# Kernel optimization log

Hardware: AMD Instinct MI355X
Metric: run time of the kernel (lower is better)

## Reference

```python
import jax, jax.numpy as jnp
import numpy as np

B, T, D = 1, 1024, 256
NH, MULT = 4, 32
N = MULT * D // NH          # 2048 sparse dim per head
CS = 256                    # rotary chunk size
V, VP = 50257, 50304        # vocab, padded vocab
L = 4                       # n_layer (single shared BDHLayer applied L times)
GATE_DIV = 1024.0
CHUNK = 64                  # GLA chunk size
ROPE_BASE = 2.0 ** 18
SCALE_BASE = 512.0


def sqrelu(x):
    return jnp.square(jax.nn.relu(x))


def rmsnorm(x, eps=1e-5):
    return x * jax.lax.rsqrt(jnp.mean(jnp.square(x), -1, keepdims=True) + eps)


def layernorm(x, eps=1e-5):
    m = jnp.mean(x, -1, keepdims=True)
    v = jnp.var(x, -1, keepdims=True)
    return (x - m) * jax.lax.rsqrt(v + eps)


def rope_tables(t_len):
    # flash-attn RotaryEmbedding with xpos scale_base (q branch)
    inv_freq = 1.0 / (ROPE_BASE ** (jnp.arange(0, CS, 2, dtype=jnp.float32) / CS))
    t = jnp.arange(t_len, dtype=jnp.float32)
    freqs = t[:, None] * inv_freq[None, :]                       # [T, CS/2]
    xpos_scale = (jnp.arange(0, CS, 2, dtype=jnp.float32) + 0.4 * CS) / (1.4 * CS)
    power = (t - t_len // 2) / SCALE_BASE
    sc = xpos_scale[None, :] ** power[:, None]
    return jnp.cos(freqs) * sc, jnp.sin(freqs) * sc


def apply_rope(x, cos, sin):
    # x: [B, T, nchunks, CS]; non-interleaved rotation of full CS dim
    half = CS // 2
    x1, x2 = x[..., :half], x[..., half:]
    c = cos[None, :, None, :]
    s = sin[None, :, None, :]
    return jnp.concatenate([x1 * c - x2 * s, x2 * c + x1 * s], axis=-1)


def chunk_gla(q, k, v, g):
    # Gated linear attention: S_t = exp(g_t)[:,None]*S_{t-1} + k_t v_t^T; o_t = scale*q_t @ S_t
    # q,k,g: [B,T,H,N] (g = log decay <= 0), v: [B,T,H,Dv]. Chunked, IO-aware form.
    Bq, Tq, H, Nk = q.shape
    Dv = v.shape[-1]
    nc = Tq // CHUNK
    scale = Nk ** -0.5  # fla default scale = K**-0.5

    def to_chunks(x):
        return x.reshape(Bq, nc, CHUNK, H, -1).transpose(1, 0, 3, 2, 4)  # [nc,B,H,C,*]

    qc, kc, vc, gc = to_chunks(q), to_chunks(k), to_chunks(v), to_chunks(g)
    mask = jnp.tril(jnp.ones((CHUNK, CHUNK), dtype=q.dtype))

    def step(S, inp):
        qb, kb, vb, gb = inp                              # [B,H,C,N], v: [B,H,C,Dv]
        gcs = jnp.cumsum(gb, axis=2)                      # inclusive cumulative log-decay
        qg = qb * jnp.exp(gcs) * scale
        A = jnp.einsum('bhtn,bhsn->bhts', qg, kb * jnp.exp(-gcs))
        o = jnp.einsum('bhts,bhsd->bhtd', A * mask, vb)   # intra-chunk
        o = o + jnp.einsum('bhtn,bhnd->bhtd', qg, S)      # inter-chunk
        g_last = gcs[:, :, -1, :]                         # [B,H,N]
        kS = kb * jnp.exp(g_last[:, :, None, :] - gcs)
        S = S * jnp.exp(g_last)[..., None] + jnp.einsum('bhtn,bhtd->bhnd', kS, vb)
        return S, o

    S0 = jnp.zeros((Bq, H, Nk, Dv), dtype=q.dtype)
    _, outs = jax.lax.scan(step, S0, (qc, kc, vc, gc))    # outs: [nc,B,H,C,Dv]
    return outs.transpose(1, 0, 3, 2, 4).reshape(Bq, Tq, H, Dv)


def bdh_layer(x, enc_w, enc_gate_w, dec_w, enc_v_w, cos, sin):
    Bx, Tx, Dx = x.shape
    xs = sqrelu(x @ enc_w.T)                              # [B,T,NH*N] sparse activations
    xr = apply_rope(xs.reshape(Bx, Tx, -1, CS), cos, sin)
    q = xr.reshape(Bx, Tx, NH, N)
    gate = sqrelu(x @ enc_gate_w.T).reshape(Bx, Tx, NH, N) / GATE_DIV
    v = jnp.broadcast_to(x[:, :, None, :], (Bx, Tx, NH, Dx))
    o = chunk_gla(q, q, v, -gate)                         # K = Q, g = -gate
    o = layernorm(o)                                      # middle_norm (no affine)
    ys = sqrelu(jnp.einsum('bthd,hnd->bthn', o, enc_v_w)) # per-head encoder_v
    xy = (xs.reshape(Bx, Tx, NH, N) * ys).reshape(Bx, Tx, NH * N)
    y = layernorm(xy @ dec_w.T)                           # end_norm (no affine)
    return rmsnorm(y + x)


def setup_inputs() -> dict:
    key = jax.random.key(0)
    ks = jax.random.split(key, 7)
    std = 0.02
    return {
        'embed_w': jax.random.normal(ks[0], (VP, D), jnp.float32) * std,
        'lm_head_w': jax.random.normal(ks[1], (VP, D), jnp.float32) * std,
        'enc_w': jax.random.normal(ks[2], (NH * N, D), jnp.float32) * std,
        'enc_gate_w': jax.random.normal(ks[3], (NH * N, D), jnp.float32) * std,
        'dec_w': jax.random.normal(ks[4], (D, NH * N), jnp.float32) * std,
        'enc_v_w': jax.random.normal(ks[5], (NH, N, D), jnp.float32) * std,
        'backout_lambda': 0.2 * jnp.ones((1,), jnp.float32),
        'resid_lambdas': jnp.ones((L,), jnp.float32),
        'x0_lambdas': jnp.zeros((L,), jnp.float32),
        'idx': jax.random.randint(ks[6], (B, T), 0, V, dtype=jnp.int32),
    }


def reference(embed_w, lm_head_w, enc_w, enc_gate_w, dec_w, enc_v_w,
              backout_lambda, resid_lambdas, x0_lambdas, idx):
    cos, sin = rope_tables(T)
    x = rmsnorm(embed_w[idx])                             # [B,T,D]
    x0 = x
    for i in range(L):                                    # single shared layer applied L times
        xin = resid_lambdas[i] * x + x0_lambdas[i] * x0
        x = bdh_layer(xin, enc_w, enc_gate_w, dec_w, enc_v_w, cos, sin)
    x = rmsnorm(x - backout_lambda * x0)                  # backout of embedding direction
    return x @ lm_head_w.T                                # logits [B,T,VP]
```

## Files before the change

kernel.cpp:

```cpp
#include <hip/hip_runtime.h>
#include <math.h>

#define TLEN 1024
#define DDIM 256
#define NH_  4
#define NDIM 2048
#define HN   8192
#define NCH  16
#define CHK  64
#define VP_  50304
#define SCALE_Q 0.022097086912079608f

typedef unsigned short u16;
typedef __attribute__((ext_vector_type(8))) short short8;
typedef __attribute__((ext_vector_type(4))) float f32x4;

#define MFMA16(a,b,c) __builtin_amdgcn_mfma_f32_16x16x32_bf16((a),(b),(c),0,0,0)

__device__ __forceinline__ float bf2f(u16 u){ return __uint_as_float(((unsigned)u)<<16); }
__device__ __forceinline__ u16 f2bf(float f){
  unsigned x = __float_as_uint(f);
  return (u16)((x + 0x7fffu + ((x>>16)&1u)) >> 16);
}
__device__ __forceinline__ float wave_sum(float v){
  #pragma unroll
  for(int o=1;o<64;o<<=1) v += __shfl_xor(v,o,64);
  return v;
}
__device__ __forceinline__ float block_sum(float v, float* tmp){
  v = wave_sum(v);
  __syncthreads();
  if((threadIdx.x&63)==0) tmp[threadIdx.x>>6]=v;
  __syncthreads();
  return tmp[0]+tmp[1]+tmp[2]+tmp[3];
}

__device__ __forceinline__ void gload16(const u16* g, u16* l){
  __builtin_amdgcn_global_load_lds((const __attribute__((address_space(1))) unsigned int*)g,
                                   (__attribute__((address_space(3))) unsigned int*)l, 16, 0, 0);
}
__device__ __forceinline__ short8 frag_lin(const u16* lds, int row, int k){
  return *(const short8*)((const char*)lds + row*128 + k*2);
}
__device__ __forceinline__ short8 frag64(const u16* lds, int row, int k){
  return *(const short8*)((const char*)lds + row*128 + ((k*2) ^ ((row&7)<<4)));
}
__device__ __forceinline__ short8 frag512(const u16* lds, int row, int k){
  return *(const short8*)((const char*)lds + row*512 + ((k*2) ^ ((row&7)<<4)));
}

__global__ __launch_bounds__(256) void k_setup(
  const float* __restrict__ emb, const int* __restrict__ idx,
  const float* rl, const float* xl,
  const float* __restrict__ enc_w, const float* __restrict__ gate_w,
  const float* __restrict__ dec_w, const float* __restrict__ encv_w,
  u16* w_enc, u16* w_gate, u16* w_dec, u16* w_encv,
  float* cosT, float* sinT, float* x0, float* xin, u16* xin_bf){
  __shared__ float tmp[4];
  int bid = blockIdx.x, tid = threadIdx.x;
  if(bid < 1024){
    if(tid < 128){
      int t = bid, i = tid;
      float inv_freq = exp2f(-18.0f * (float)(2*i) * (1.0f/256.0f));
      float fr = (float)t * inv_freq;
      float xsc = ((float)(2*i) + 102.4f) * (1.0f/358.4f);
      float power = ((float)t - 512.0f) * (1.0f/512.0f);
      float sc = exp2f(power * log2f(xsc));
      cosT[t*128+i] = cosf(fr)*sc;
      sinT[t*128+i] = sinf(fr)*sc;
    }
  } else if(bid < 5120){
    size_t base = (size_t)(bid-1024)*2048 + tid;
    #pragma unroll
    for(int k=0;k<8;k++){
      size_t i = base + (size_t)k*256;
      int seg = (int)(i>>21); size_t off = i & 2097151;
      const float* s; u16* dst;
      if(seg==0){ s=enc_w; dst=w_enc; } else if(seg==1){ s=gate_w; dst=w_gate; }
      else if(seg==2){ s=dec_w; dst=w_dec; } else { s=encv_w; dst=w_encv; }
      dst[off] = f2bf(s[off]);
    }
  } else {
    int t = bid - 5120, d = tid;
    float v = emb[(size_t)idx[t]*DDIM + d];
    float s = block_sum(v*v, tmp);
    float o = v * rsqrtf(s*(1.0f/DDIM) + 1e-5f);
    x0[t*DDIM+d] = o;
    float xi = rl[0]*o + xl[0]*o;
    xin[t*DDIM+d] = xi; xin_bf[t*DDIM+d] = f2bf(xi);
  }
}

template<bool SPLITK>
__global__ __launch_bounds__(256) void k_gemm(
  const u16* __restrict__ A, int lda, const u16* __restrict__ B, int ldb,
  float* __restrict__ C, int ldc, int kchunk)
{
  __shared__ __align__(16) u16 sA[128*64];
  __shared__ __align__(16) u16 sB[128*64];
  const int m0 = blockIdx.x*128, n0 = blockIdx.y*128;
  const int k0 = blockIdx.z*kchunk;
  const int tid = threadIdx.x, lane = tid&63, wv = tid>>6;
  const int wr = (wv>>1)*64, wc = (wv&1)*64;
  f32x4 acc[4][4];
  #pragma unroll
  for(int i=0;i<4;i++)
    #pragma unroll
    for(int j=0;j<4;j++) acc[i][j] = (f32x4){0.f,0.f,0.f,0.f};
  for(int kb=0; kb<kchunk; kb+=64){
    __syncthreads();
    #pragma unroll
    for(int p=0;p<4;p++){
      int r = p*32 + (tid>>3), cb = tid&7;
      int off = r*64 + cb*8;
      gload16(A + (size_t)(m0+r)*lda + k0+kb + cb*8, sA + off);
      gload16(B + (size_t)(n0+r)*ldb + k0+kb + cb*8, sB + off);
    }
    __syncthreads();
    #pragma unroll
    for(int ks=0;ks<2;ks++){
      short8 af[4], bfr[4];
      int kk = ks*32 + 8*(lane>>4);
      #pragma unroll
      for(int i=0;i<4;i++){
        af[i]  = frag_lin(sA, wr + i*16 + (lane&15), kk);
        bfr[i] = frag_lin(sB, wc + i*16 + (lane&15), kk);
      }
      #pragma unroll
      for(int i=0;i<4;i++)
        #pragma unroll
        for(int j=0;j<4;j++)
          acc[i][j] = MFMA16(af[i], bfr[j], acc[i][j]);
    }
  }
  size_t poff = SPLITK ? (size_t)blockIdx.z * (size_t)gridDim.x * 128 * ldc : 0;
  const int rb = 4*(lane>>4), cb2 = lane&15;
  #pragma unroll
  for(int i=0;i<4;i++)
    #pragma unroll
    for(int j=0;j<4;j++){
      int col = n0 + wc + j*16 + cb2;
      #pragma unroll
      for(int r=0;r<4;r++){
        int row = m0 + wr + i*16 + rb + r;
        C[poff + (size_t)row*ldc + col] = acc[i][j][r];
      }
    }
}

__global__ __launch_bounds__(256) void k_gemm_lm(
  const u16* __restrict__ A, const float* __restrict__ Bf, float* __restrict__ C)
{
  __shared__ __align__(16) u16 sB[128*256];
  __shared__ __align__(16) u16 sA[128*64];
  const int n0 = blockIdx.y*128, mbase = blockIdx.x*4;
  const int tid = threadIdx.x, lane = tid&63, wv = tid>>6;
  const int wr = (wv>>1)*64, wc = (wv&1)*64;
  {
    int n = tid>>1, half = tid&1;
    const float* bp = Bf + (size_t)(n0+n)*DDIM + half*128;
    #pragma unroll
    for(int s=0;s<16;s++){
      f32x4 v0 = *(const f32x4*)(bp + s*8);
      f32x4 v1 = *(const f32x4*)(bp + s*8 + 4);
      short8 w;
      #pragma unroll
      for(int e=0;e<4;e++){ w[e]=(short)f2bf(v0[e]); w[e+4]=(short)f2bf(v1[e]); }
      int k0 = half*128 + s*8;
      *(short8*)((char*)sB + n*512 + ((k0*2) ^ ((n&7)<<4))) = w;
    }
  }
  for(int mi=0; mi<4; mi++){
    int m0 = (mbase+mi)*128;
    f32x4 acc[4][4];
    #pragma unroll
    for(int i=0;i<4;i++)
      #pragma unroll
      for(int j=0;j<4;j++) acc[i][j] = (f32x4){0.f,0.f,0.f,0.f};
    for(int kb=0; kb<4; kb++){
      __syncthreads();
      #pragma unroll
      for(int p=0;p<4;p++){
        int r = p*32 + (tid>>3), cb = tid&7;
        gload16(A + (size_t)(m0+r)*DDIM + kb*64 + cb*8, sA + r*64 + cb*8);
      }
      __syncthreads();
      #pragma unroll
      for(int ks=0;ks<2;ks++){
        short8 af[4], bfr[4];
        int kk = ks*32 + 8*(lane>>4);
        #pragma unroll
        for(int i=0;i<4;i++){
          af[i]  = frag_lin(sA, wr + i*16 + (lane&15), kk);
          bfr[i] = frag512(sB, wc + i*16 + (lane&15), kb*64 + kk);
        }
        #pragma unroll
        for(int i=0;i<4;i++)
          #pragma unroll
          for(int j=0;j<4;j++)
            acc[i][j] = MFMA16(af[i], bfr[j], acc[i][j]);
      }
    }
    const int rb = 4*(lane>>4), cb2 = lane&15;
    #pragma unroll
    for(int i=0;i<4;i++)
      #pragma unroll
      for(int j=0;j<4;j++){
        int col = n0 + wc + j*16 + cb2;
        #pragma unroll
        for(int r=0;r<4;r++){
          int row = m0 + wr + i*16 + rb + r;
          C[(size_t)row*VP_ + col] = acc[i][j][r];
        }
      }
  }
}

__global__ __launch_bounds__(256) void k_gemm_eg(
  const u16* __restrict__ xin_bf, const u16* __restrict__ w_enc, const u16* __restrict__ w_gate,
  u16* __restrict__ xs, u16* __restrict__ gate)
{
  __shared__ __align__(16) u16 sA[128*64];
  __shared__ __align__(16) u16 sB[128*64];
  const int yy = blockIdx.y;
  const bool isg = yy >= 64;
  const u16* B = isg ? w_gate : w_enc;
  u16* C = isg ? gate : xs;
  const float mul = isg ? (1.0f/1024.0f) : 1.0f;
  const int m0 = blockIdx.x*128, n0 = (yy&63)*128;
  const int tid = threadIdx.x, lane = tid&63, wv = tid>>6;
  const int wr = (wv>>1)*64, wc = (wv&1)*64;
  f32x4 acc[4][4];
  #pragma unroll
  for(int i=0;i<4;i++)
    #pragma unroll
    for(int j=0;j<4;j++) acc[i][j] = (f32x4){0.f,0.f,0.f,0.f};
  for(int kb=0; kb<DDIM; kb+=64){
    __syncthreads();
    #pragma unroll
    for(int p=0;p<4;p++){
      int r = p*32 + (tid>>3), cb = tid&7;
      int off = r*64 + cb*8;
      gload16(xin_bf + (size_t)(m0+r)*DDIM + kb + cb*8, sA + off);
      gload16(B + (size_t)(n0+r)*DDIM + kb + cb*8, sB + off);
    }
    __syncthreads();
    #pragma unroll
    for(int ks=0;ks<2;ks++){
      short8 af[4], bfr[4];
      int kk = ks*32 + 8*(lane>>4);
      #pragma unroll
      for(int i=0;i<4;i++){
        af[i]  = frag_lin(sA, wr + i*16 + (lane&15), kk);
        bfr[i] = frag_lin(sB, wc + i*16 + (lane&15), kk);
      }
      #pragma unroll
      for(int i=0;i<4;i++)
        #pragma unroll
        for(int j=0;j<4;j++)
          acc[i][j] = MFMA16(af[i], bfr[j], acc[i][j]);
    }
  }
  const int rb = 4*(lane>>4), cb2 = lane&15;
  #pragma unroll
  for(int i=0;i<4;i++)
    #pragma unroll
    for(int j=0;j<4;j++){
      int col = n0 + wc + j*16 + cb2;
      #pragma unroll
      for(int r=0;r<4;r++){
        int row = m0 + wr + i*16 + rb + r;
        float v = acc[i][j][r];
        float a = v>0.f ? v*v*mul : 0.f;
        C[(size_t)row*HN + col] = f2bf(a);
      }
    }
}

__global__ __launch_bounds__(256) void k_gemm_ys(
  const u16* __restrict__ olnp, const u16* __restrict__ wvp,
  const u16* __restrict__ xs, u16* __restrict__ xy)
{
  __shared__ __align__(16) u16 sA[128*64];
  __shared__ __align__(16) u16 sB[128*64];
  const int m0 = blockIdx.x*128, n0 = blockIdx.y*128, h = blockIdx.z;
  const u16* A = olnp + (size_t)h*TLEN*DDIM;
  const u16* B = wvp  + (size_t)h*NDIM*DDIM;
  const int tid = threadIdx.x, lane = tid&63, wv = tid>>6;
  const int wr = (wv>>1)*64, wc = (wv&1)*64;
  f32x4 acc[4][4];
  #pragma unroll
  for(int i=0;i<4;i++)
    #pragma unroll
    for(int j=0;j<4;j++) acc[i][j] = (f32x4){0.f,0.f,0.f,0.f};
  for(int kb=0; kb<DDIM; kb+=64){
    __syncthreads();
    #pragma unroll
    for(int p=0;p<4;p++){
      int r = p*32 + (tid>>3), cb = tid&7;
      int off = r*64 + cb*8;
      gload16(A + (size_t)(m0+r)*DDIM + kb + cb*8, sA + off);
      gload16(B + (size_t)(n0+r)*DDIM + kb + cb*8, sB + off);
    }
    __syncthreads();
    #pragma unroll
    for(int ks=0;ks<2;ks++){
      short8 af[4], bfr[4];
      int kk = ks*32 + 8*(lane>>4);
      #pragma unroll
      for(int i=0;i<4;i++){
        af[i]  = frag_lin(sA, wr + i*16 + (lane&15), kk);
        bfr[i] = frag_lin(sB, wc + i*16 + (lane&15), kk);
      }
      #pragma unroll
      for(int i=0;i<4;i++)
        #pragma unroll
        for(int j=0;j<4;j++)
          acc[i][j] = MFMA16(af[i], bfr[j], acc[i][j]);
    }
  }
  const int rb = 4*(lane>>4), cb2 = lane&15;
  #pragma unroll
  for(int i=0;i<4;i++)
    #pragma unroll
    for(int j=0;j<4;j++){
      int col = h*NDIM + n0 + wc + j*16 + cb2;
      #pragma unroll
      for(int r=0;r<4;r++){
        int row = m0 + wr + i*16 + rb + r;
        float v = acc[i][j][r];
        float a = v>0.f ? v*v : 0.f;
        a *= bf2f(xs[(size_t)row*HN + col]);
        xy[(size_t)row*HN + col] = f2bf(a);
      }
    }
}

__global__ __launch_bounds__(256) void k_phase_a(const u16* __restrict__ xs, u16* __restrict__ gate,
                          const float* __restrict__ cosT, const float* __restrict__ sinT,
                          u16* __restrict__ qg, u16* __restrict__ kgT, float* __restrict__ gle,
                          const u16* __restrict__ xin_bf, u16* __restrict__ vbT){
  __shared__ u16 s[64*DDIM];
  int c = blockIdx.y;
  if(blockIdx.x == 32){
    int tid = threadIdx.x;
    #pragma unroll
    for(int p=0;p<8;p++){
      int idx = p*256+tid; int t = idx>>5, cb = idx&31;
      *(short8*)(s + t*DDIM + cb*8) = *(const short8*)(xin_bf + ((size_t)c*CHK + t)*DDIM + cb*8);
    }
    __syncthreads();
    int d = tid;
    u16 col[64];
    #pragma unroll
    for(int t=0;t<64;t++) col[t] = s[t*DDIM + d];
    u16* dst = vbT + ((size_t)c*DDIM + d)*CHK;
    #pragma unroll
    for(int p=0;p<8;p++){
      short8 v;
      #pragma unroll
      for(int e=0;e<8;e++) v[e] = (short)col[p*8+e];
      *(short8*)(dst + p*8) = v;
    }
    return;
  }
  int j = blockIdx.x*256 + threadIdx.x;
  int h = j>>11, n = j&2047;
  int cc = j & 255;
  int ci = cc & 127;
  bool hi_ = cc >= 128;
  int poff = hi_ ? -128 : 128;
  size_t base = (size_t)c*CHK*HN + j;
  float gsum = 0.f;
  #pragma unroll
  for(int t=0;t<CHK;t++) gsum -= bf2f(gate[base + (size_t)t*HN]);
  float egsum = expf(gsum);
  u16 kv[64];
  float gc = 0.f;
  #pragma unroll
  for(int t=0;t<CHK;t++){
    size_t ix = base + (size_t)t*HN;
    gc -= bf2f(gate[ix]);
    int tt = c*CHK + t;
    float own = bf2f(xs[ix]), oth = bf2f(xs[ix + poff]);
    float cs = cosT[tt*128+ci], sn = sinT[tt*128+ci];
    float qv = hi_ ? (own*cs + oth*sn) : (own*cs - oth*sn);
    float e1 = expf(gc);
    qg[ix] = f2bf(qv * e1 * SCALE_Q);
    u16 kgv = f2bf(qv / e1);
    gate[ix] = kgv;
    kv[t] = kgv;
  }
  u16* kb = kgT + (((size_t)c*NH_ + h)*NDIM + n)*CHK;
  #pragma unroll
  for(int p=0;p<8;p++){
    short8 v;
    #pragma unroll
    for(int e=0;e<8;e++) v[e] = (short)kv[p*8+e];
    *(short8*)(kb + p*8) = v;
  }
  gle[(size_t)c*HN + j] = egsum;
}

__global__ __launch_bounds__(256) void k_qk_part(const u16* __restrict__ qg, const u16* __restrict__ kg,
                                                 float* __restrict__ Apart){
  int c = blockIdx.x, h = blockIdx.y, kz = blockIdx.z;
  int tid = threadIdx.x, lane = tid&63, wv = tid>>6;
  __shared__ __align__(16) u16 sQ[2][64*64], sK[2][64*64];
  const u16* qb = qg + (size_t)c*CHK*HN + h*NDIM + kz*512;
  const u16* kb = kg + (size_t)c*CHK*HN + h*NDIM + kz*512;
  f32x4 acc[4];
  #pragma unroll
  for(int j=0;j<4;j++) acc[j] = (f32x4){0.f,0.f,0.f,0.f};
  #pragma unroll
  for(int p=0;p<2;p++){
    int r = p*32 + (tid>>3), cb = tid&7;
    int off = r*64 + cb*8;
    gload16(qb + (size_t)r*HN + cb*8, sQ[0] + off);
    gload16(kb + (size_t)r*HN + cb*8, sK[0] + off);
  }
  __syncthreads();
  for(int kt=0; kt<8; kt++){
    if(kt<7){
      #pragma unroll
      for(int p=0;p<2;p++){
        int r = p*32 + (tid>>3), cb = tid&7;
        int off = r*64 + cb*8;
        gload16(qb + (kt+1)*64 + (size_t)r*HN + cb*8, sQ[(kt+1)&1] + off);
        gload16(kb + (kt+1)*64 + (size_t)r*HN + cb*8, sK[(kt+1)&1] + off);
      }
    }
    #pragma unroll
    for(int kh=0;kh<2;kh++){
      int kk = kh*32 + 8*(lane>>4);
      short8 af = frag_lin(sQ[kt&1], wv*16 + (lane&15), kk);
      #pragma unroll
      for(int j=0;j<4;j++){
        short8 b = frag_lin(sK[kt&1], j*16 + (lane&15), kk);
        acc[j] = MFMA16(af, b, acc[j]);
      }
    }
    __syncthreads();
  }
  int rb = 4*(lane>>4), cl = lane&15;
  float* ab = Apart + (size_t)kz*(NCH*NH_*4096) + ((size_t)c*NH_+h)*4096;
  #pragma unroll
  for(int j=0;j<4;j++)
    #pragma unroll
    for(int r=0;r<4;r++){
      int t = wv*16 + rb + r, s = j*16 + cl;
      ab[t*64 + s] = acc[j][r];
    }
}

__global__ __launch_bounds__(256) void k_state(const u16* __restrict__ kgT, const u16* __restrict__ vbT,
                                               const float* __restrict__ gle, u16* __restrict__ ST){
  int nb = blockIdx.x, db = blockIdx.y, h = blockIdx.z;
  int tid = threadIdx.x, lane = tid&63, wv = tid>>6;
  __shared__ __align__(16) u16 sK[2][32*64], sV[2][64*64];
  __shared__ __align__(16) u16 sD[64*32];
  int ng = nb*32;
  int r8a = tid>>3, cb = tid&7;
  f32x4 S[2];
  S[0] = (f32x4){0.f,0.f,0.f,0.f}; S[1] = (f32x4){0.f,0.f,0.f,0.f};
  gload16(kgT + (((size_t)0*NH_ + h)*NDIM + ng + r8a)*CHK + cb*8, sK[0] + r8a*64 + cb*8);
  #pragma unroll
  for(int p=0;p<2;p++){
    int r = p*32 + r8a;
    gload16(vbT + ((size_t)0*DDIM + db*64 + r)*CHK + cb*8, sV[0] + r*64 + cb*8);
  }
  int cur = 0;
  for(int c=0;c<15;c++){
    __syncthreads();
    if(c<14){
      gload16(kgT + (((size_t)(c+1)*NH_ + h)*NDIM + ng + r8a)*CHK + cb*8, sK[cur^1] + r8a*64 + cb*8);
      #pragma unroll
      for(int p=0;p<2;p++){
        int r = p*32 + r8a;
        gload16(vbT + ((size_t)(c+1)*DDIM + db*64 + r)*CHK + cb*8, sV[cur^1] + r*64 + cb*8);
      }
    }
    #pragma unroll
    for(int kh=0;kh<2;kh++){
      int kk = kh*32 + 8*(lane>>4);
      short8 af = frag_lin(sV[cur], wv*16 + (lane&15), kk);
      #pragma unroll
      for(int fn=0;fn<2;fn++){
        short8 b = frag_lin(sK[cur], fn*16 + (lane&15), kk);
        S[fn] = MFMA16(af, b, S[fn]);
      }
    }
    #pragma unroll
    for(int fn=0;fn<2;fn++){
      float gv = gle[(size_t)c*HN + h*NDIM + ng + fn*16 + (lane&15)];
      S[fn][0]*=gv; S[fn][1]*=gv; S[fn][2]*=gv; S[fn][3]*=gv;
    }
    #pragma unroll
    for(int fn=0;fn<2;fn++)
      #pragma unroll
      for(int r=0;r<4;r++){
        int d = wv*16 + 4*(lane>>4) + r, n = fn*16 + (lane&15);
        *(u16*)((char*)sD + d*64 + ((n*2) ^ (((d>>2)&3)<<4))) = f2bf(S[fn][r]);
      }
    __syncthreads();
    {
      int dl = tid>>2, seg = tid&3;
      short8 v = *(const short8*)((const char*)sD + dl*64 + ((seg*16) ^ (((dl>>2)&3)<<4)));
      *(short8*)(ST + (((size_t)c*NH_ + h)*DDIM + db*64 + dl)*NDIM + ng + seg*8) = v;
    }
    cur ^= 1;
  }
}

__global__ __launch_bounds__(256) void k_out(const u16* __restrict__ qg, const u16* __restrict__ ST,
                                             const float* __restrict__ Apart, const u16* __restrict__ vbT,
                                             float* __restrict__ op){
  int c = blockIdx.x, h = blockIdx.y, zz = blockIdx.z;
  int db = zz>>1, nz = zz&1;
  int tid = threadIdx.x, lane = tid&63, wv = tid>>6;
  __shared__ __align__(16) u16 sQ[2][64*64], sS[2][64*64];
  __shared__ __align__(16) u16 sAm[64*64], sV[64*64];
  const u16* stb = (c>0) ? ST + ((size_t)(c-1)*NH_ + h)*DDIM*(size_t)NDIM + (size_t)db*64*NDIM : ST;
  const u16* qb  = qg + (size_t)c*CHK*HN + h*NDIM;
  const int ktA = nz ? 15 : 0, ktB = nz ? 32 : 15;
  int r8a = tid>>3, cb = tid&7;
  f32x4 acc[4];
  #pragma unroll
  for(int j=0;j<4;j++) acc[j] = (f32x4){0.f,0.f,0.f,0.f};
  if(c>0){
    #pragma unroll
    for(int p=0;p<2;p++){
      int r = p*32 + r8a;
      gload16(qb + ktA*64 + (size_t)r*HN + cb*8, sQ[0] + r*64 + cb*8);
      gload16(stb + (size_t)r*NDIM + ktA*64 + cb*8, sS[0] + r*64 + cb*8);
    }
  }
  if(nz==0){
    size_t abase = ((size_t)c*NH_ + h)*4096;
    #pragma unroll
    for(int e=0;e<16;e++){
      int idx = e*256 + tid;
      int t = idx>>6, s = idx&63;
      float sum = Apart[abase + idx]
                + Apart[(size_t)(NCH*NH_*4096)   + abase + idx]
                + Apart[(size_t)(NCH*NH_*4096)*2 + abase + idx]
                + Apart[(size_t)(NCH*NH_*4096)*3 + abase + idx];
      *(u16*)((char*)sAm + t*128 + ((s*2)^((t&7)<<4))) = f2bf((s<=t)? sum : 0.f);
    }
    #pragma unroll
    for(int p=0;p<2;p++){
      int r = p*32 + r8a;
      gload16(vbT + ((size_t)c*DDIM + db*64 + r)*CHK + cb*8, sV + r*64 + cb*8);
    }
  }
  __syncthreads();
  if(nz==0){
    #pragma unroll
    for(int kh=0;kh<2;kh++){
      int kk = kh*32 + 8*(lane>>4);
      short8 af = frag64(sAm, wv*16 + (lane&15), kk);
      #pragma unroll
      for(int j=0;j<4;j++){
        short8 b = frag_lin(sV, j*16 + (lane&15), kk);
        acc[j] = MFMA16(af, b, acc[j]);
      }
    }
  }
  if(c>0){
    int cur = 0;
    for(int kt=ktA; kt<ktB; kt++){
      if(kt+1<ktB){
        #pragma unroll
        for(int p=0;p<2;p++){
          int r = p*32 + r8a;
          gload16(qb + (kt+1)*64 + (size_t)r*HN + cb*8, sQ[cur^1] + r*64 + cb*8);
          gload16(stb + (size_t)r*NDIM + (kt+1)*64 + cb*8, sS[cur^1] + r*64 + cb*8);
        }
      }
      #pragma unroll
      for(int kh=0;kh<2;kh++){
        int kk = kh*32 + 8*(lane>>4);
        short8 af = frag_lin(sQ[cur], wv*16 + (lane&15), kk);
        #pragma unroll
        for(int j=0;j<4;j++){
          short8 b = frag_lin(sS[cur], j*16 + (lane&15), kk);
          acc[j] = MFMA16(af, b, acc[j]);
        }
      }
      __syncthreads();
      cur ^= 1;
    }
  }
  int rb = 4*(lane>>4), cl = lane&15;
  #pragma unroll
  for(int j=0;j<4;j++){
    int d = db*64 + j*16 + cl;
    #pragma unroll
    for(int r=0;r<4;r++){
      int t = c*CHK + wv*16 + rb + r;
      op[((size_t)(nz*NH_ + h)*TLEN + t)*DDIM + d] = acc[j][r];
    }
  }
}

__global__ __launch_bounds__(256) void k_ln(const float* __restrict__ op, u16* __restrict__ oln){
  __shared__ float tmp[4];
  int t = blockIdx.x, h = blockIdx.y, d = threadIdx.x;
  size_t ix = ((size_t)h*TLEN + t)*DDIM + d;
  float v = op[ix] + op[(size_t)NH_*TLEN*DDIM + ix];
  float s1 = block_sum(v, tmp);
  float m = s1*(1.0f/DDIM);
  float cv = v - m;
  float s2 = block_sum(cv*cv, tmp);
  oln[ix] = f2bf(cv * rsqrtf(s2*(1.0f/DDIM) + 1e-5f));
}

__global__ __launch_bounds__(256) void k_post(const float* __restrict__ ypart, float* __restrict__ xin,
                                              const float* __restrict__ x0,
                                              const float* rl, const float* xl, const float* bl,
                                              int li, u16* __restrict__ xin_bf, u16* __restrict__ xf){
  __shared__ float tmp[4];
  int t = blockIdx.x, d = threadIdx.x;
  float v = 0.f;
  #pragma unroll
  for(int z=0;z<16;z++) v += ypart[(size_t)z*TLEN*DDIM + t*DDIM + d];
  float s1 = block_sum(v, tmp);
  float m = s1*(1.0f/DDIM);
  float cvt = v - m;
  float s2 = block_sum(cvt*cvt, tmp);
  float y = cvt * rsqrtf(s2*(1.0f/DDIM) + 1e-5f);
  float xn = y + xin[t*DDIM+d];
  float s3 = block_sum(xn*xn, tmp);
  float xv = xn * rsqrtf(s3*(1.0f/DDIM) + 1e-5f);
  if(li<3){
    float xi = rl[li+1]*xv + xl[li+1]*x0[t*DDIM+d];
    xin[t*DDIM+d] = xi; xin_bf[t*DDIM+d] = f2bf(xi);
  } else {
    float fv = xv - bl[0]*x0[t*DDIM+d];
    float s4 = block_sum(fv*fv, tmp);
    xf[t*DDIM+d] = f2bf(fv * rsqrtf(s4*(1.0f/DDIM) + 1e-5f));
  }
}

extern "C" void kernel_launch(void* const* d_in, const int* in_sizes, int n_in,
                              void* d_out, int out_size, void* d_ws, size_t ws_size,
                              hipStream_t stream){
  (void)in_sizes; (void)n_in; (void)out_size; (void)ws_size;
  const float* embed_w = (const float*)d_in[0];
  const float* lm_w    = (const float*)d_in[1];
  const float* enc_w   = (const float*)d_in[2];
  const float* gate_w  = (const float*)d_in[3];
  const float* dec_w   = (const float*)d_in[4];
  const float* encv_w  = (const float*)d_in[5];
  const float* backout = (const float*)d_in[6];
  const float* rlam    = (const float*)d_in[7];
  const float* xlam    = (const float*)d_in[8];
  const int*   idx     = (const int*)d_in[9];
  float* out = (float*)d_out;

  char* p = (char*)d_ws;
  auto alloc = [&](size_t b)->char*{ char* r=p; p += (b+255)&~(size_t)255; return r; };
  float* cosT = (float*)alloc((size_t)TLEN*128*4);
  float* sinT = (float*)alloc((size_t)TLEN*128*4);
  float* x0   = (float*)alloc((size_t)TLEN*DDIM*4);
  float* xin  = (float*)alloc((size_t)TLEN*DDIM*4);
  u16* xin_bf = (u16*)alloc((size_t)TLEN*DDIM*2);
  u16* xs     = (u16*)alloc((size_t)TLEN*HN*2);
  u16* q      = (u16*)alloc((size_t)TLEN*HN*2);
  u16* gate   = (u16*)alloc((size_t)TLEN*HN*2);
  (void)alloc((size_t)15*NH_*DDIM*NDIM*2 - (size_t)TLEN*HN*2);
  u16* ST     = gate;
  float* ypart= (float*)xs;
  u16* kgT    = (u16*)alloc((size_t)NCH*NH_*NDIM*CHK*2);
  float* gle  = (float*)alloc((size_t)NCH*HN*4);
  u16* vbT    = (u16*)alloc((size_t)NCH*DDIM*CHK*2);
  float* Apart= (float*)alloc((size_t)4*NCH*NH_*CHK*CHK*4);
  float* op   = (float*)alloc((size_t)2*NH_*TLEN*DDIM*4);
  u16* oln    = (u16*)alloc((size_t)NH_*TLEN*DDIM*2);
  u16* xf     = (u16*)alloc((size_t)TLEN*DDIM*2);
  u16* w_enc  = (u16*)alloc((size_t)HN*DDIM*2);
  u16* w_gate = (u16*)alloc((size_t)HN*DDIM*2);
  u16* w_dec  = (u16*)alloc((size_t)DDIM*HN*2);
  u16* w_encv = (u16*)alloc((size_t)NH_*NDIM*DDIM*2);

  k_setup<<<6144,256,0,stream>>>(embed_w, idx, rlam, xlam,
                                 enc_w, gate_w, dec_w, encv_w,
                                 w_enc, w_gate, w_dec, w_encv,
                                 cosT, sinT, x0, xin, xin_bf);

  for(int li=0; li<4; li++){
    k_gemm_eg<<<dim3(8,128),256,0,stream>>>(xin_bf,w_enc,w_gate,xs,gate);
    k_phase_a<<<dim3(33,NCH),256,0,stream>>>(xs,gate,cosT,sinT,q,kgT,gle,xin_bf,vbT);
    k_qk_part<<<dim3(NCH,NH_,4),256,0,stream>>>(q,gate,Apart);
    k_state<<<dim3(64,4,NH_),256,0,stream>>>(kgT,vbT,gle,ST);
    k_out<<<dim3(NCH,NH_,8),256,0,stream>>>(q,ST,Apart,vbT,op);
    k_ln<<<dim3(TLEN,NH_),256,0,stream>>>(op,oln);
    k_gemm_ys<<<dim3(8,16,NH_),256,0,stream>>>(oln,w_encv,xs,q);
    k_gemm<true><<<dim3(8,2,16),256,0,stream>>>(q,HN,w_dec,HN,ypart,DDIM,512);
    k_post<<<TLEN,256,0,stream>>>(ypart,xin,x0,rlam,xlam,backout,li,xin_bf,xf);
  }
  k_gemm_lm<<<dim3(2,393),256,0,stream>>>(xf, lm_w, out);
}
```

Before: 700.8 us.

## Keep full-K weight tile resident in LDS and loop over four M tiles

In the encoder/gate GEMM and the ys GEMM, each block now loads its 128x256 weight tile once into swizzled LDS and reuses it across four consecutive 128-row M tiles, instead of reloading weights per block. The grid shrinks by 4x in the M dimension. This cuts global weight traffic and LDS staging of B, but it lowers block count (256 and 128 blocks), which may underfill the GPU. It also uses about 80KB of LDS per block, which limits occupancy, and the weight load is a synchronous preload.

```diff
diff --git a/kernel.cpp b/kernel.cpp
--- a/kernel.cpp
+++ b/kernel.cpp
@@ -220,120 +220,142 @@
   const u16* __restrict__ xin_bf, const u16* __restrict__ w_enc, const u16* __restrict__ w_gate,
   u16* __restrict__ xs, u16* __restrict__ gate)
 {
+  __shared__ __align__(16) u16 sB[128*256];
   __shared__ __align__(16) u16 sA[128*64];
-  __shared__ __align__(16) u16 sB[128*64];
   const int yy = blockIdx.y;
   const bool isg = yy >= 64;
   const u16* B = isg ? w_gate : w_enc;
   u16* C = isg ? gate : xs;
   const float mul = isg ? (1.0f/1024.0f) : 1.0f;
-  const int m0 = blockIdx.x*128, n0 = (yy&63)*128;
+  const int n0 = (yy&63)*128, mbase = blockIdx.x*4;
   const int tid = threadIdx.x, lane = tid&63, wv = tid>>6;
   const int wr = (wv>>1)*64, wc = (wv&1)*64;
-  f32x4 acc[4][4];
-  #pragma unroll
-  for(int i=0;i<4;i++)
-    #pragma unroll
-    for(int j=0;j<4;j++) acc[i][j] = (f32x4){0.f,0.f,0.f,0.f};
-  for(int kb=0; kb<DDIM; kb+=64){
-    __syncthreads();
-    #pragma unroll
-    for(int p=0;p<4;p++){
-      int r = p*32 + (tid>>3), cb = tid&7;
-      int off = r*64 + cb*8;
-      gload16(xin_bf + (size_t)(m0+r)*DDIM + kb + cb*8, sA + off);
-      gload16(B + (size_t)(n0+r)*DDIM + kb + cb*8, sB + off);
-    }
-    __syncthreads();
-    #pragma unroll
-    for(int ks=0;ks<2;ks++){
-      short8 af[4], bfr[4];
-      int kk = ks*32 + 8*(lane>>4);
-      #pragma unroll
-      for(int i=0;i<4;i++){
-        af[i]  = frag_lin(sA, wr + i*16 + (lane&15), kk);
-        bfr[i] = frag_lin(sB, wc + i*16 + (lane&15), kk);
-      }
-      #pragma unroll
-      for(int i=0;i<4;i++)
-        #pragma unroll
-        for(int j=0;j<4;j++)
-          acc[i][j] = MFMA16(af[i], bfr[j], acc[i][j]);
-    }
-  }
-  const int rb = 4*(lane>>4), cb2 = lane&15;
-  #pragma unroll
-  for(int i=0;i<4;i++)
-    #pragma unroll
-    for(int j=0;j<4;j++){
-      int col = n0 + wc + j*16 + cb2;
-      #pragma unroll
-      for(int r=0;r<4;r++){
-        int row = m0 + wr + i*16 + rb + r;
-        float v = acc[i][j][r];
-        float a = v>0.f ? v*v*mul : 0.f;
-        C[(size_t)row*HN + col] = f2bf(a);
-      }
-    }
+  {
+    int n = tid>>1, half = tid&1;
+    const u16* bp = B + (size_t)(n0+n)*DDIM + half*128;
+    #pragma unroll
+    for(int s=0;s<16;s++){
+      short8 w = *(const short8*)(bp + s*8);
+      int k0 = half*128 + s*8;
+      *(short8*)((char*)sB + n*512 + ((k0*2) ^ ((n&7)<<4))) = w;
+    }
+  }
+  for(int mi=0; mi<4; mi++){
+    int m0 = (mbase+mi)*128;
+    f32x4 acc[4][4];
+    #pragma unroll
+    for(int i=0;i<4;i++)
+      #pragma unroll
+      for(int j=0;j<4;j++) acc[i][j] = (f32x4){0.f,0.f,0.f,0.f};
+    for(int kb=0; kb<4; kb++){
+      __syncthreads();
+      #pragma unroll
+      for(int p=0;p<4;p++){
+        int r = p*32 + (tid>>3), cb = tid&7;
+        gload16(xin_bf + (size_t)(m0+r)*DDIM + kb*64 + cb*8, sA + r*64 + cb*8);
+      }
+      __syncthreads();
+      #pragma unroll
+      for(int ks=0;ks<2;ks++){
+        short8 af[4], bfr[4];
+        int kk = ks*32 + 8*(lane>>4);
+        #pragma unroll
+        for(int i=0;i<4;i++){
+          af[i]  = frag_lin(sA, wr + i*16 + (lane&15), kk);
+          bfr[i] = frag512(sB, wc + i*16 + (lane&15), kb*64 + kk);
+        }
+        #pragma unroll
+        for(int i=0;i<4;i++)
+          #pragma unroll
+          for(int j=0;j<4;j++)
+            acc[i][j] = MFMA16(af[i], bfr[j], acc[i][j]);
+      }
+    }
+    const int rb = 4*(lane>>4), cb2 = lane&15;
+    #pragma unroll
+    for(int i=0;i<4;i++)
+      #pragma unroll
+      for(int j=0;j<4;j++){
+        int col = n0 + wc + j*16 + cb2;
+        #pragma unroll
+        for(int r=0;r<4;r++){
+          int row = m0 + wr + i*16 + rb + r;
+          float v = acc[i][j][r];
+          float a = v>0.f ? v*v*mul : 0.f;
+          C[(size_t)row*HN + col] = f2bf(a);
+        }
+      }
+  }
 }
 
 __global__ __launch_bounds__(256) void k_gemm_ys(
   const u16* __restrict__ olnp, const u16* __restrict__ wvp,
   const u16* __restrict__ xs, u16* __restrict__ xy)
 {
+  __shared__ __align__(16) u16 sB[128*256];
   __shared__ __align__(16) u16 sA[128*64];
-  __shared__ __align__(16) u16 sB[128*64];
-  const int m0 = blockIdx.x*128, n0 = blockIdx.y*128, h = blockIdx.z;
+  const int n0 = blockIdx.y*128, h = blockIdx.z, mbase = blockIdx.x*4;
   const u16* A = olnp + (size_t)h*TLEN*DDIM;
   const u16* B = wvp  + (size_t)h*NDIM*DDIM;
   const int tid = threadIdx.x, lane = tid&63, wv = tid>>6;
   const int wr = (wv>>1)*64, wc = (wv&1)*64;
-  f32x4 acc[4][4];
-  #pragma unroll
-  for(int i=0;i<4;i++)
-    #pragma unroll
-    for(int j=0;j<4;j++) acc[i][j] = (f32x4){0.f,0.f,0.f,0.f};
-  for(int kb=0; kb<DDIM; kb+=64){
-    __syncthreads();
-    #pragma unroll
-    for(int p=0;p<4;p++){
-      int r = p*32 + (tid>>3), cb = tid&7;
-      int off = r*64 + cb*8;
-      gload16(A + (size_t)(m0+r)*DDIM + kb + cb*8, sA + off);
-      gload16(B + (size_t)(n0+r)*DDIM + kb + cb*8, sB + off);
-    }
-    __syncthreads();
-    #pragma unroll
-    for(int ks=0;ks<2;ks++){
-      short8 af[4], bfr[4];
-      int kk = ks*32 + 8*(lane>>4);
-      #pragma unroll
-      for(int i=0;i<4;i++){
-        af[i]  = frag_lin(sA, wr + i*16 + (lane&15), kk);
-        bfr[i] = frag_lin(sB, wc + i*16 + (lane&15), kk);
-      }
-      #pragma unroll
-      for(int i=0;i<4;i++)
-        #pragma unroll
-        for(int j=0;j<4;j++)
-          acc[i][j] = MFMA16(af[i], bfr[j], acc[i][j]);
-    }
-  }
-  const int rb = 4*(lane>>4), cb2 = lane&15;
-  #pragma unroll
-  for(int i=0;i<4;i++)
-    #pragma unroll
-    for(int j=0;j<4;j++){
-      int col = h*NDIM + n0 + wc + j*16 + cb2;
-      #pragma unroll
-      for(int r=0;r<4;r++){
-        int row = m0 + wr + i*16 + rb + r;
-        float v = acc[i][j][r];
-        float a = v>0.f ? v*v : 0.f;
-        a *= bf2f(xs[(size_t)row*HN + col]);
-        xy[(size_t)row*HN + col] = f2bf(a);
-      }
-    }
+  {
+    int n = tid>>1, half = tid&1;
+    const u16* bp = B + (size_t)(n0+n)*DDIM + half*128;
+    #pragma unroll
+    for(int s=0;s<16;s++){
+      short8 w = *(const short8*)(bp + s*8);
+      int k0 = half*128 + s*8;
+      *(short8*)((char*)sB + n*512 + ((k0*2) ^ ((n&7)<<4))) = w;
+    }
+  }
+  for(int mi=0; mi<4; mi++){
+    int m0 = (mbase+mi)*128;
+    f32x4 acc[4][4];
+    #pragma unroll
+    for(int i=0;i<4;i++)
+      #pragma unroll
+      for(int j=0;j<4;j++) acc[i][j] = (f32x4){0.f,0.f,0.f,0.f};
+    for(int kb=0; kb<4; kb++){
+      __syncthreads();
+      #pragma unroll
+      for(int p=0;p<4;p++){
+        int r = p*32 + (tid>>3), cb = tid&7;
+        gload16(A + (size_t)(m0+r)*DDIM + kb*64 + cb*8, sA + r*64 + cb*8);
+      }
+      __syncthreads();
+      #pragma unroll
+      for(int ks=0;ks<2;ks++){
+        short8 af[4], bfr[4];
+        int kk = ks*32 + 8*(lane>>4);
+        #pragma unroll
+        for(int i=0;i<4;i++){
+          af[i]  = frag_lin(sA, wr + i*16 + (lane&15), kk);
+          bfr[i] = frag512(sB, wc + i*16 + (lane&15), kb*64 + kk);
+        }
+        #pragma unroll
+        for(int i=0;i<4;i++)
+          #pragma unroll
+          for(int j=0;j<4;j++)
+            acc[i][j] = MFMA16(af[i], bfr[j], acc[i][j]);
+      }
+    }
+    const int rb = 4*(lane>>4), cb2 = lane&15;
+    #pragma unroll
+    for(int i=0;i<4;i++)
+      #pragma unroll
+      for(int j=0;j<4;j++){
+        int col = h*NDIM + n0 + wc + j*16 + cb2;
+        #pragma unroll
+        for(int r=0;r<4;r++){
+          int row = m0 + wr + i*16 + rb + r;
+          float v = acc[i][j][r];
+          float a = v>0.f ? v*v : 0.f;
+          a *= bf2f(xs[(size_t)row*HN + col]);
+          xy[(size_t)row*HN + col] = f2bf(a);
+        }
+      }
+  }
 }
 
 __global__ __launch_bounds__(256) void k_phase_a(const u16* __restrict__ xs, u16* __restrict__ gate,
@@ -689,13 +711,13 @@
                                  cosT, sinT, x0, xin, xin_bf);
 
   for(int li=0; li<4; li++){
-    k_gemm_eg<<<dim3(8,128),256,0,stream>>>(xin_bf,w_enc,w_gate,xs,gate);
+    k_gemm_eg<<<dim3(2,128),256,0,stream>>>(xin_bf,w_enc,w_gate,xs,gate);
     k_phase_a<<<dim3(33,NCH),256,0,stream>>>(xs,gate,cosT,sinT,q,kgT,gle,xin_bf,vbT);
     k_qk_part<<<dim3(NCH,NH_,4),256,0,stream>>>(q,gate,Apart);
     k_state<<<dim3(64,4,NH_),256,0,stream>>>(kgT,vbT,gle,ST);
     k_out<<<dim3(NCH,NH_,8),256,0,stream>>>(q,ST,Apart,vbT,op);
     k_ln<<<dim3(TLEN,NH_),256,0,stream>>>(op,oln);
-    k_gemm_ys<<<dim3(8,16,NH_),256,0,stream>>>(oln,w_encv,xs,q);
+    k_gemm_ys<<<dim3(2,16,NH_),256,0,stream>>>(oln,w_encv,xs,q);
     k_gemm<true><<<dim3(8,2,16),256,0,stream>>>(q,HN,w_dec,HN,ypart,DDIM,512);
     k_post<<<TLEN,256,0,stream>>>(ypart,xin,x0,rlam,xlam,backout,li,xin_bf,xf);
   }
```

Result: slower. 884.8 us (+26.3%).

## Merge QK-partial and state kernels, read gated keys directly without transposed copy

Applied to the files above, without the earlier changes.

The phase-A kernel no longer writes a transposed per-chunk copy of the gated keys (kgT). The state kernel now loads keys straight from the row-major gate buffer and transposes them through swizzled shared memory. It is merged with the QK-partial kernel into a single launch, with the first 256 blocks doing QK and the rest doing state. This cuts a large extra write/read of the key tensor and one launch, and lets the two independent jobs overlap. In exchange, ST gets its own allocation instead of aliasing gate, so workspace grows, and the key loads are narrower strided row reads.

```diff
diff --git a/kernel.cpp b/kernel.cpp
--- a/kernel.cpp
+++ b/kernel.cpp
@@ -338,7 +338,7 @@
 
 __global__ __launch_bounds__(256) void k_phase_a(const u16* __restrict__ xs, u16* __restrict__ gate,
                           const float* __restrict__ cosT, const float* __restrict__ sinT,
-                          u16* __restrict__ qg, u16* __restrict__ kgT, float* __restrict__ gle,
+                          u16* __restrict__ qg, float* __restrict__ gle,
                           const u16* __restrict__ xin_bf, u16* __restrict__ vbT){
   __shared__ u16 s[64*DDIM];
   int c = blockIdx.y;
@@ -365,7 +365,6 @@
     return;
   }
   int j = blockIdx.x*256 + threadIdx.x;
-  int h = j>>11, n = j&2047;
   int cc = j & 255;
   int ci = cc & 127;
   bool hi_ = cc >= 128;
@@ -375,7 +374,6 @@
   #pragma unroll
   for(int t=0;t<CHK;t++) gsum -= bf2f(gate[base + (size_t)t*HN]);
   float egsum = expf(gsum);
-  u16 kv[64];
   float gc = 0.f;
   #pragma unroll
   for(int t=0;t<CHK;t++){
@@ -387,128 +385,125 @@
     float qv = hi_ ? (own*cs + oth*sn) : (own*cs - oth*sn);
     float e1 = expf(gc);
     qg[ix] = f2bf(qv * e1 * SCALE_Q);
-    u16 kgv = f2bf(qv / e1);
-    gate[ix] = kgv;
-    kv[t] = kgv;
-  }
-  u16* kb = kgT + (((size_t)c*NH_ + h)*NDIM + n)*CHK;
-  #pragma unroll
-  for(int p=0;p<8;p++){
-    short8 v;
-    #pragma unroll
-    for(int e=0;e<8;e++) v[e] = (short)kv[p*8+e];
-    *(short8*)(kb + p*8) = v;
+    gate[ix] = f2bf(qv / e1);
   }
   gle[(size_t)c*HN + j] = egsum;
 }
 
-__global__ __launch_bounds__(256) void k_qk_part(const u16* __restrict__ qg, const u16* __restrict__ kg,
-                                                 float* __restrict__ Apart){
-  int c = blockIdx.x, h = blockIdx.y, kz = blockIdx.z;
+__global__ __launch_bounds__(256) void k_qk_state(
+  const u16* __restrict__ qg, const u16* __restrict__ kg, float* __restrict__ Apart,
+  const u16* __restrict__ vbT, const float* __restrict__ gle, u16* __restrict__ ST){
+  __shared__ __align__(16) u16 smem[16384];
+  int bid = blockIdx.x;
   int tid = threadIdx.x, lane = tid&63, wv = tid>>6;
-  __shared__ __align__(16) u16 sQ[2][64*64], sK[2][64*64];
-  const u16* qb = qg + (size_t)c*CHK*HN + h*NDIM + kz*512;
-  const u16* kb = kg + (size_t)c*CHK*HN + h*NDIM + kz*512;
-  f32x4 acc[4];
-  #pragma unroll
-  for(int j=0;j<4;j++) acc[j] = (f32x4){0.f,0.f,0.f,0.f};
-  #pragma unroll
-  for(int p=0;p<2;p++){
-    int r = p*32 + (tid>>3), cb = tid&7;
-    int off = r*64 + cb*8;
-    gload16(qb + (size_t)r*HN + cb*8, sQ[0] + off);
-    gload16(kb + (size_t)r*HN + cb*8, sK[0] + off);
-  }
-  __syncthreads();
-  for(int kt=0; kt<8; kt++){
-    if(kt<7){
-      #pragma unroll
-      for(int p=0;p<2;p++){
-        int r = p*32 + (tid>>3), cb = tid&7;
-        int off = r*64 + cb*8;
-        gload16(qb + (kt+1)*64 + (size_t)r*HN + cb*8, sQ[(kt+1)&1] + off);
-        gload16(kb + (kt+1)*64 + (size_t)r*HN + cb*8, sK[(kt+1)&1] + off);
-      }
-    }
-    #pragma unroll
-    for(int kh=0;kh<2;kh++){
-      int kk = kh*32 + 8*(lane>>4);
-      short8 af = frag_lin(sQ[kt&1], wv*16 + (lane&15), kk);
-      #pragma unroll
-      for(int j=0;j<4;j++){
-        short8 b = frag_lin(sK[kt&1], j*16 + (lane&15), kk);
-        acc[j] = MFMA16(af, b, acc[j]);
-      }
-    }
-    __syncthreads();
-  }
-  int rb = 4*(lane>>4), cl = lane&15;
-  float* ab = Apart + (size_t)kz*(NCH*NH_*4096) + ((size_t)c*NH_+h)*4096;
-  #pragma unroll
-  for(int j=0;j<4;j++)
-    #pragma unroll
-    for(int r=0;r<4;r++){
-      int t = wv*16 + rb + r, s = j*16 + cl;
-      ab[t*64 + s] = acc[j][r];
-    }
-}
-
-__global__ __launch_bounds__(256) void k_state(const u16* __restrict__ kgT, const u16* __restrict__ vbT,
-                                               const float* __restrict__ gle, u16* __restrict__ ST){
-  int nb = blockIdx.x, db = blockIdx.y, h = blockIdx.z;
-  int tid = threadIdx.x, lane = tid&63, wv = tid>>6;
-  __shared__ __align__(16) u16 sK[2][32*64], sV[2][64*64];
-  __shared__ __align__(16) u16 sD[64*32];
-  int ng = nb*32;
-  int r8a = tid>>3, cb = tid&7;
-  f32x4 S[2];
-  S[0] = (f32x4){0.f,0.f,0.f,0.f}; S[1] = (f32x4){0.f,0.f,0.f,0.f};
-  gload16(kgT + (((size_t)0*NH_ + h)*NDIM + ng + r8a)*CHK + cb*8, sK[0] + r8a*64 + cb*8);
-  #pragma unroll
-  for(int p=0;p<2;p++){
-    int r = p*32 + r8a;
-    gload16(vbT + ((size_t)0*DDIM + db*64 + r)*CHK + cb*8, sV[0] + r*64 + cb*8);
-  }
-  int cur = 0;
-  for(int c=0;c<15;c++){
-    __syncthreads();
-    if(c<14){
-      gload16(kgT + (((size_t)(c+1)*NH_ + h)*NDIM + ng + r8a)*CHK + cb*8, sK[cur^1] + r8a*64 + cb*8);
-      #pragma unroll
-      for(int p=0;p<2;p++){
-        int r = p*32 + r8a;
-        gload16(vbT + ((size_t)(c+1)*DDIM + db*64 + r)*CHK + cb*8, sV[cur^1] + r*64 + cb*8);
-      }
-    }
-    #pragma unroll
-    for(int kh=0;kh<2;kh++){
-      int kk = kh*32 + 8*(lane>>4);
-      short8 af = frag_lin(sV[cur], wv*16 + (lane&15), kk);
+  if(bid < 256){
+    int c = bid&15, h = (bid>>4)&3, kz = bid>>6;
+    const u16* qb = qg + (size_t)c*CHK*HN + h*NDIM + kz*512;
+    const u16* kb = kg + (size_t)c*CHK*HN + h*NDIM + kz*512;
+    f32x4 acc[4];
+    #pragma unroll
+    for(int j=0;j<4;j++) acc[j] = (f32x4){0.f,0.f,0.f,0.f};
+    #pragma unroll
+    for(int p=0;p<2;p++){
+      int r = p*32 + (tid>>3), cb = tid&7;
+      int off = r*64 + cb*8;
+      gload16(qb + (size_t)r*HN + cb*8, smem + off);
+      gload16(kb + (size_t)r*HN + cb*8, smem + 8192 + off);
+    }
+    __syncthreads();
+    for(int kt=0; kt<8; kt++){
+      int curo = (kt&1)*4096, nxto = ((kt+1)&1)*4096;
+      if(kt<7){
+        #pragma unroll
+        for(int p=0;p<2;p++){
+          int r = p*32 + (tid>>3), cb = tid&7;
+          int off = r*64 + cb*8;
+          gload16(qb + (kt+1)*64 + (size_t)r*HN + cb*8, smem + nxto + off);
+          gload16(kb + (kt+1)*64 + (size_t)r*HN + cb*8, smem + 8192 + nxto + off);
+        }
+      }
+      #pragma unroll
+      for(int kh=0;kh<2;kh++){
+        int kk = kh*32 + 8*(lane>>4);
+        short8 af = frag_lin(smem + curo, wv*16 + (lane&15), kk);
+        #pragma unroll
+        for(int j=0;j<4;j++){
+          short8 b = frag_lin(smem + 8192 + curo, j*16 + (lane&15), kk);
+          acc[j] = MFMA16(af, b, acc[j]);
+        }
+      }
+      __syncthreads();
+    }
+    int rb = 4*(lane>>4), cl = lane&15;
+    float* ab = Apart + (size_t)kz*(NCH*NH_*4096) + ((size_t)c*NH_+h)*4096;
+    #pragma unroll
+    for(int j=0;j<4;j++)
+      #pragma unroll
+      for(int r=0;r<4;r++){
+        int t = wv*16 + rb + r, s = j*16 + cl;
+        ab[t*64 + s] = acc[j][r];
+      }
+  } else {
+    int idx = bid - 256;
+    int nb = idx&63, db = (idx>>6)&3, h = idx>>8;
+    int ng = nb*32;
+    int r8a = tid>>3, cb = tid&7;
+    int tr = tid>>2, tseg = tid&3;
+    f32x4 S[2];
+    S[0] = (f32x4){0.f,0.f,0.f,0.f}; S[1] = (f32x4){0.f,0.f,0.f,0.f};
+    short8 kreg = *(const short8*)(kg + (size_t)tr*HN + h*NDIM + ng + tseg*8);
+    #pragma unroll
+    for(int p=0;p<2;p++){
+      int r = p*32 + r8a;
+      gload16(vbT + ((size_t)0*DDIM + db*64 + r)*CHK + cb*8, smem + 4096 + r*64 + cb*8);
+    }
+    int cur = 0;
+    for(int c=0;c<15;c++){
+      #pragma unroll
+      for(int e=0;e<8;e++){
+        int n = tseg*8 + e;
+        *(u16*)((char*)smem + cur*4096 + n*128 + ((tr*2) ^ ((n&7)<<4))) = (u16)kreg[e];
+      }
+      __syncthreads();
+      if(c<14){
+        kreg = *(const short8*)(kg + (size_t)((c+1)*CHK + tr)*HN + h*NDIM + ng + tseg*8);
+        int nxt = cur^1;
+        #pragma unroll
+        for(int p=0;p<2;p++){
+          int r = p*32 + r8a;
+          gload16(vbT + ((size_t)(c+1)*DDIM + db*64 + r)*CHK + cb*8, smem + 4096 + nxt*4096 + r*64 + cb*8);
+        }
+      }
+      #pragma unroll
+      for(int kh=0;kh<2;kh++){
+        int kk = kh*32 + 8*(lane>>4);
+        short8 af = frag_lin(smem + 4096 + cur*4096, wv*16 + (lane&15), kk);
+        #pragma unroll
+        for(int fn=0;fn<2;fn++){
+          short8 b = frag64(smem + cur*2048, fn*16 + (lane&15), kk);
+          S[fn] = MFMA16(af, b, S[fn]);
+        }
+      }
       #pragma unroll
       for(int fn=0;fn<2;fn++){
-        short8 b = frag_lin(sK[cur], fn*16 + (lane&15), kk);
-        S[fn] = MFMA16(af, b, S[fn]);
-      }
-    }
-    #pragma unroll
-    for(int fn=0;fn<2;fn++){
-      float gv = gle[(size_t)c*HN + h*NDIM + ng + fn*16 + (lane&15)];
-      S[fn][0]*=gv; S[fn][1]*=gv; S[fn][2]*=gv; S[fn][3]*=gv;
-    }
-    #pragma unroll
-    for(int fn=0;fn<2;fn++)
-      #pragma unroll
-      for(int r=0;r<4;r++){
-        int d = wv*16 + 4*(lane>>4) + r, n = fn*16 + (lane&15);
-        *(u16*)((char*)sD + d*64 + ((n*2) ^ (((d>>2)&3)<<4))) = f2bf(S[fn][r]);
-      }
-    __syncthreads();
-    {
-      int dl = tid>>2, seg = tid&3;
-      short8 v = *(const short8*)((const char*)sD + dl*64 + ((seg*16) ^ (((dl>>2)&3)<<4)));
-      *(short8*)(ST + (((size_t)c*NH_ + h)*DDIM + db*64 + dl)*NDIM + ng + seg*8) = v;
-    }
-    cur ^= 1;
+        float gv = gle[(size_t)c*HN + h*NDIM + ng + fn*16 + (lane&15)];
+        S[fn][0]*=gv; S[fn][1]*=gv; S[fn][2]*=gv; S[fn][3]*=gv;
+      }
+      #pragma unroll
+      for(int fn=0;fn<2;fn++)
+        #pragma unroll
+        for(int r=0;r<4;r++){
+          int d = wv*16 + 4*(lane>>4) + r, n = fn*16 + (lane&15);
+          *(u16*)((char*)(smem + 12288) + d*64 + ((n*2) ^ (((d>>2)&3)<<4))) = f2bf(S[fn][r]);
+        }
+      __syncthreads();
+      {
+        int dl = tid>>2, seg = tid&3;
+        short8 v = *(const short8*)((const char*)(smem + 12288) + dl*64 + ((seg*16) ^ (((dl>>2)&3)<<4)));
+        *(short8*)(ST + (((size_t)c*NH_ + h)*DDIM + db*64 + dl)*NDIM + ng + seg*8) = v;
+      }
+      cur ^= 1;
+    }
   }
 }
 
@@ -668,10 +663,8 @@
   u16* xs     = (u16*)alloc((size_t)TLEN*HN*2);
   u16* q      = (u16*)alloc((size_t)TLEN*HN*2);
   u16* gate   = (u16*)alloc((size_t)TLEN*HN*2);
-  (void)alloc((size_t)15*NH_*DDIM*NDIM*2 - (size_t)TLEN*HN*2);
-  u16* ST     = gate;
+  u16* ST     = (u16*)alloc((size_t)15*NH_*DDIM*NDIM*2);
   float* ypart= (float*)xs;
-  u16* kgT    = (u16*)alloc((size_t)NCH*NH_*NDIM*CHK*2);
   float* gle  = (float*)alloc((size_t)NCH*HN*4);
   u16* vbT    = (u16*)alloc((size_t)NCH*DDIM*CHK*2);
   float* Apart= (float*)alloc((size_t)4*NCH*NH_*CHK*CHK*4);
@@ -690,9 +683,8 @@
 
   for(int li=0; li<4; li++){
     k_gemm_eg<<<dim3(8,128),256,0,stream>>>(xin_bf,w_enc,w_gate,xs,gate);
-    k_phase_a<<<dim3(33,NCH),256,0,stream>>>(xs,gate,cosT,sinT,q,kgT,gle,xin_bf,vbT);
-    k_qk_part<<<dim3(NCH,NH_,4),256,0,stream>>>(q,gate,Apart);
-    k_state<<<dim3(64,4,NH_),256,0,stream>>>(kgT,vbT,gle,ST);
+    k_phase_a<<<dim3(33,NCH),256,0,stream>>>(xs,gate,cosT,sinT,q,gle,xin_bf,vbT);
+    k_qk_state<<<1280,256,0,stream>>>(q,gate,Apart,vbT,gle,ST);
     k_out<<<dim3(NCH,NH_,8),256,0,stream>>>(q,ST,Apart,vbT,op);
     k_ln<<<dim3(TLEN,NH_),256,0,stream>>>(op,oln);
     k_gemm_ys<<<dim3(8,16,NH_),256,0,stream>>>(oln,w_encv,xs,q);
```

New measurement: 646.8 us. 1.08x faster.
